# Kernel optimization log

Measured on AMD Instinct MI355X. Metric: run time of the kernel, lower is better.

## Reference

```python
import itertools
import jax, jax.numpy as jnp
import numpy as np

GRID = (41, 1600, 1408)   # KITTI voxel grid (z, y, x)
N_VOX = 80000
C_IN, C_OUT = 32, 64
NEG_SLOPE = 0.01          # nn.LeakyReLU default
BN_EPS = 1e-5

# ---------- numpy rulebook construction (spconv indice pairs) ----------

def _lin(c, grid):
    return (c[:, 0] * grid[1] + c[:, 1]) * grid[2] + c[:, 2]

def _lookup(lin_sorted, q, valid):
    pos = np.searchsorted(lin_sorted, q)
    pos = np.clip(pos, 0, len(lin_sorted) - 1)
    found = valid & (lin_sorted[pos] == q)
    return np.where(found, pos, len(lin_sorted)).astype(np.int32)  # sentinel = N

def _offsets(kshape, d):
    rs = [([-d, 0, d] if s == 3 else [0]) for s in kshape]
    return list(itertools.product(*rs))

def _subm_map(coords, lin_sorted, grid, kshape, d):
    offs = _offsets(kshape, d)
    g = np.asarray(grid)
    nbr = np.empty((len(offs), len(coords)), np.int32)
    for k, off in enumerate(offs):
        q = coords + np.asarray(off)
        valid = ((q >= 0) & (q < g)).all(1)
        nbr[k] = _lookup(lin_sorted, _lin(q, grid), valid)
    return nbr

def _build_maps(seed=0):
    rng = np.random.default_rng(seed)
    tot = GRID[0] * GRID[1] * GRID[2]
    lin0 = np.sort(rng.choice(tot, size=N_VOX, replace=False))
    c0 = np.stack(np.unravel_index(lin0, GRID), axis=1).astype(np.int64)
    nbr331_d1 = _subm_map(c0, lin0, GRID, (3, 3, 1), 1)
    nbr313_d1 = _subm_map(c0, lin0, GRID, (3, 1, 3), 1)
    # SparseConv3d k=3 s=2 p=1: output active sites = union over inputs/offsets
    og = tuple((g + 2 - 3) // 2 + 1 for g in GRID)
    offs27 = np.asarray(list(itertools.product(range(3), repeat=3)))
    cand = c0[None, :, :] + 1 - offs27[:, None, :]
    ok = (cand % 2 == 0).all(-1)
    p = cand // 2
    ok &= ((p >= 0) & (p < np.asarray(og))).all(-1)
    plin = (p[..., 0] * og[1] + p[..., 1]) * og[2] + p[..., 2]
    lin1 = np.unique(plin[ok])
    c1 = np.stack(np.unravel_index(lin1, og), axis=1).astype(np.int64)
    M = len(c1)
    pool_nbr = np.empty((27, M), np.int32)
    gg = np.asarray(GRID)
    for k in range(27):
        q = c1 * 2 - 1 + offs27[k]
        valid = ((q >= 0) & (q < gg)).all(1)
        pool_nbr[k] = _lookup(lin0, _lin(q, GRID), valid)
    nbr331_d2 = _subm_map(c1, lin1, og, (3, 3, 1), 2)
    nbr313_d2 = _subm_map(c1, lin1, og, (3, 1, 3), 2)
    nbr331_d3 = _subm_map(c1, lin1, og, (3, 3, 1), 3)
    nbr313_d3 = _subm_map(c1, lin1, og, (3, 1, 3), 3)
    maps = dict(nbr331_d1=jnp.asarray(nbr331_d1), nbr313_d1=jnp.asarray(nbr313_d1),
                pool_nbr=jnp.asarray(pool_nbr), nbr331_d2=jnp.asarray(nbr331_d2),
                nbr313_d2=jnp.asarray(nbr313_d2), nbr331_d3=jnp.asarray(nbr331_d3),
                nbr313_d3=jnp.asarray(nbr313_d3))
    return maps, M

# ---------- jax forward ----------

def _subm(f, nbr, W):
    # gather-GEMM-scatter sparse conv: out[n] = sum_k f[nbr[k,n]] @ W[k]
    padf = jnp.concatenate([f, jnp.zeros((1, f.shape[1]), f.dtype)], 0)  # zero row for missing nbr
    out = jnp.zeros((nbr.shape[1], W.shape[2]), f.dtype)
    for k in range(nbr.shape[0]):  # fixed small kernel-volume loop (9 or 27)
        out = out + padf[nbr[k]] @ W[k]
    return out

def _bn_act(x):
    # BatchNorm1d (training stats, gamma=1, beta=0 per weight_initialization) + LeakyReLU
    m = jnp.mean(x, 0)
    v = jnp.var(x, 0)
    return jax.nn.leaky_relu((x - m) * jax.lax.rsqrt(v + BN_EPS), NEG_SLOPE)

def _res(f, nA, nB, w1, w12, w2, w22):
    # nA: (3,3,1) map (conv3x1), nB: (3,1,3) map (conv1x3)
    s = _bn_act(_subm(f, nA, w1))
    s = _bn_act(_subm(s, nB, w12))
    r = _bn_act(_subm(f, nB, w2))
    r = _bn_act(_subm(r, nA, w22))
    return r + s

def setup_inputs() -> dict:
    maps, M = _build_maps()
    ks = jax.random.split(jax.random.key(0), 16)
    def w(k, shape):
        fan = shape[-2] * (shape[0] if len(shape) == 3 else 1)
        return jax.random.normal(k, shape, jnp.float32) / np.sqrt(fan)
    inp = dict(
        feats=jax.random.normal(ks[0], (N_VOX, C_IN), jnp.float32),
        b1_w1=w(ks[1], (9, C_IN, C_OUT)), b1_w1_2=w(ks[2], (9, C_OUT, C_OUT)),
        b1_w2=w(ks[3], (9, C_IN, C_OUT)), b1_w2_2=w(ks[4], (9, C_OUT, C_OUT)),
        pool_w=w(ks[5], (27, C_OUT, C_OUT)),
        b2_w1=w(ks[6], (9, C_OUT, C_OUT)), b2_w1_2=w(ks[7], (9, C_OUT, C_OUT)),
        b2_w2=w(ks[8], (9, C_OUT, C_OUT)), b2_w2_2=w(ks[9], (9, C_OUT, C_OUT)),
        b3_w1=w(ks[10], (9, C_OUT, C_OUT)), b3_w1_2=w(ks[11], (9, C_OUT, C_OUT)),
        b3_w2=w(ks[12], (9, C_OUT, C_OUT)), b3_w2_2=w(ks[13], (9, C_OUT, C_OUT)),
        down_w=w(ks[14], (3 * C_OUT, C_OUT)),
    )
    inp.update(maps)
    return inp

def reference(feats, b1_w1, b1_w1_2, b1_w2, b1_w2_2, pool_w,
              b2_w1, b2_w1_2, b2_w2, b2_w2_2,
              b3_w1, b3_w1_2, b3_w2, b3_w2_2, down_w,
              nbr331_d1, nbr313_d1, pool_nbr,
              nbr331_d2, nbr313_d2, nbr331_d3, nbr313_d3):
    x1 = _res(feats, nbr331_d1, nbr313_d1, b1_w1, b1_w1_2, b1_w2, b1_w2_2)
    x1 = _subm(x1, pool_nbr, pool_w)                     # strided SparseConv3d pool -> [M, C]
    x2 = _res(x1, nbr331_d2, nbr313_d2, b2_w1, b2_w1_2, b2_w2, b2_w2_2)  # dilation 2
    x3 = _res(x2, nbr331_d3, nbr313_d3, b3_w1, b3_w1_2, b3_w2, b3_w2_2)  # dilation 3
    return jnp.concatenate([x1, x2, x3], -1) @ down_w     # 1x1 subm conv fuse
```

## Files before the change

kernel.cpp:

```cpp
#include <hip/hip_runtime.h>
#include <hip/hip_bf16.h>

#define NEG 0.01f
#define BN_EPS 1e-5f

typedef __hip_bfloat16 bf16;
typedef __attribute__((ext_vector_type(8))) short short8;
typedef __attribute__((ext_vector_type(16))) float f32x16;

__device__ __forceinline__ float b2f(short s) {
    unsigned u = ((unsigned)(unsigned short)s) << 16;
    float f;
    __builtin_memcpy(&f, &u, 4);
    return f;
}
__device__ __forceinline__ short f2b(float f) {
    union { bf16 b; short s; } t;
    t.b = __float2bfloat16(f);
    return t.s;
}

__global__ void finalize2_k(const float* __restrict__ sA, const float* __restrict__ sB,
                            float* __restrict__ fA, float* __restrict__ fB,
                            float inv_n) {
    const float* s = blockIdx.x == 0 ? sA : sB;
    float* f = blockIdx.x == 0 ? fA : fB;
    int c = threadIdx.x;
    float sm = 0.f, sq = 0.f;
    #pragma unroll
    for (int k = 0; k < 32; ++k) {
        sm += s[k * 256 + c];
        sq += s[k * 256 + 64 + c];
    }
    float m = sm * inv_n;
    float v = sq * inv_n - m * m;
    f[c] = m;
    f[64 + c] = rsqrtf(v + BN_EPS);
}


__global__ __launch_bounds__(256) void bnact2_k(
    bf16* __restrict__ xa, const float* __restrict__ fa,
    bf16* __restrict__ xb, const float* __restrict__ fb, int nvec) {
    int i = blockIdx.x * blockDim.x + threadIdx.x;
    if (i >= 2 * nvec) return;
    bf16* x; const float* f; int j;
    if (i < nvec) { x = xa; f = fa; j = i; }
    else          { x = xb; f = fb; j = i - nvec; }
    const int c0 = (j & 7) << 3;
    short8 v = *reinterpret_cast<const short8*>(x + ((size_t)j << 3));
    short8 o;
    #pragma unroll
    for (int e = 0; e < 8; ++e) {
        float t = (b2f(v[e]) - f[c0 + e]) * f[64 + c0 + e];
        t = t > 0.f ? t : NEG * t;
        o[e] = f2b(t);
    }
    *reinterpret_cast<short8*>(x + ((size_t)j << 3)) = o;
}

__global__ __launch_bounds__(256) void bnadd_k(
    const bf16* __restrict__ a, const float* __restrict__ fa,
    const bf16* __restrict__ b, const float* __restrict__ fb,
    bf16* __restrict__ out, int nvec) {
    int i = blockIdx.x * blockDim.x + threadIdx.x;
    if (i >= nvec) return;
    const int c0 = (i & 7) << 3;
    short8 va = *reinterpret_cast<const short8*>(a + ((size_t)i << 3));
    short8 vb = *reinterpret_cast<const short8*>(b + ((size_t)i << 3));
    short8 o;
    #pragma unroll
    for (int e = 0; e < 8; ++e) {
        float ta = (b2f(va[e]) - fa[c0 + e]) * fa[64 + c0 + e];
        ta = ta > 0.f ? ta : NEG * ta;
        float tb = (b2f(vb[e]) - fb[c0 + e]) * fb[64 + c0 + e];
        tb = tb > 0.f ? tb : NEG * tb;
        o[e] = f2b(ta + tb);
    }
    *reinterpret_cast<short8*>(out + ((size_t)i << 3)) = o;
}

__global__ void cvt_f32_bf16_k(const float* __restrict__ x, bf16* __restrict__ y, int n) {
    int i = blockIdx.x * blockDim.x + threadIdx.x;
    if (i < n) y[i] = __float2bfloat16(x[i]);
}

struct PackEnt { const float* src; bf16* dst; int kt; int ns; };
struct PackArgs { PackEnt e[16]; };

__global__ void pack_w_k(PackArgs pa) {
    PackEnt E = pa.e[blockIdx.y];
    int cin = E.ns * 16;
    int total = E.kt * E.ns * 1024;
    for (int i = blockIdx.x * blockDim.x + threadIdx.x; i < total;
         i += gridDim.x * blockDim.x) {
        int j = i & 7, lane = (i >> 3) & 63, c = (i >> 9) & 1;
        int rem = i >> 10;
        int s = rem % E.ns, k = rem / E.ns;
        int krow = s * 16 + ((lane >> 5) << 3) + j;
        int col = c * 32 + (lane & 31);
        E.dst[i] = __float2bfloat16(E.src[((size_t)k * cin + krow) * 64 + col]);
    }
}

struct Job {
    const bf16* fin; const int* nbr; const bf16* Wp; bf16* out; float* stat;
    int n_out, n_in;
};
struct Jobs { Job j[2]; int t_split, t_total; };

template <int NS, int K>
__global__ __launch_bounds__(256, 6) void mconv3(Jobs jb) {
    const int CIN = NS * 16;
    const int lane = threadIdx.x & 63;
    const int col = lane & 31;
    const int q = lane >> 5;

    const int nb = gridDim.x;
    const int qq = nb >> 3, rr = nb & 7;
    const int xcd = blockIdx.x & 7, bi = blockIdx.x >> 3;
    const int sb = (xcd < rr) ? xcd * (qq + 1) + bi
                              : rr * (qq + 1) + (xcd - rr) * qq + bi;

    const int wid = sb * (blockDim.x >> 6) + (threadIdx.x >> 6);
    const int nw = gridDim.x * (blockDim.x >> 6);

    for (int tg = wid; tg < jb.t_total; tg += nw) {
        const int jsel = (tg >= jb.t_split) ? 1 : 0;
        const Job J = jb.j[jsel];
        const int tile = tg - (jsel ? jb.t_split : 0);
        const int rbase = tile << 5;
        const int r = rbase + col;
        const bool rowok = r < J.n_out;

        f32x16 acc0, acc1;
        #pragma unroll
        for (int i = 0; i < 16; ++i) { acc0[i] = 0.f; acc1[i] = 0.f; }

        #pragma unroll
        for (int g = 0; g < K / 9; ++g) {
            int idx[9];
            #pragma unroll
            for (int t = 0; t < 9; ++t)
                idx[t] = rowok ? J.nbr[(size_t)(g * 9 + t) * J.n_out + r] : J.n_in;

            #pragma unroll 1
            for (int t = 0; t < 9; ++t) {
                const bool v = idx[t] < J.n_in;
                if (__ballot(v) == 0ull) continue;
                const int k = g * 9 + t;
                const bf16* src = J.fin + (size_t)idx[t] * CIN + q * 8;
                const short8* wp = (const short8*)J.Wp + (size_t)k * (NS * 128) + lane;
                #pragma unroll
                for (int s = 0; s < NS; ++s) {
                    short8 a;
                    if (v) a = *(const short8*)(src + s * 16);
                    else { short8 z = {0,0,0,0,0,0,0,0}; a = z; }
                    short8 b0 = wp[(s * 2 + 0) * 64];
                    short8 b1 = wp[(s * 2 + 1) * 64];
                    acc0 = __builtin_amdgcn_mfma_f32_32x32x16_bf16(a, b0, acc0, 0, 0, 0);
                    acc1 = __builtin_amdgcn_mfma_f32_32x32x16_bf16(a, b1, acc1, 0, 0, 0);
                }
            }
        }

        float s0 = 0.f, q0 = 0.f, s1 = 0.f, q1 = 0.f;
        #pragma unroll
        for (int i = 0; i < 16; ++i) {
            int row = (i & 3) + 8 * (i >> 2) + 4 * q;
            int gr = rbase + row;
            if (gr < J.n_out) {
                float v0 = acc0[i], v1 = acc1[i];
                J.out[(size_t)gr * 64 + col] = __float2bfloat16(v0);
                J.out[(size_t)gr * 64 + 32 + col] = __float2bfloat16(v1);
                s0 += v0; q0 += v0 * v0;
                s1 += v1; q1 += v1 * v1;
            }
        }
        if (J.stat != nullptr) {
            s0 += __shfl_xor(s0, 32); q0 += __shfl_xor(q0, 32);
            s1 += __shfl_xor(s1, 32); q1 += __shfl_xor(q1, 32);
            float* st = J.stat + ((wid & 31) << 8);
            if (q == 0) {
                atomicAdd(&st[col], s0);
                atomicAdd(&st[64 + col], q0);
            } else {
                atomicAdd(&st[32 + col], s1);
                atomicAdd(&st[96 + col], q1);
            }
        }
    }
}

__global__ __launch_bounds__(256, 6) void down_k(
    const bf16* __restrict__ x1, const bf16* __restrict__ x2,
    const bf16* __restrict__ x3, const bf16* __restrict__ W1,
    const bf16* __restrict__ W2, const bf16* __restrict__ W3,
    float* __restrict__ out, int m) {
    const int lane = threadIdx.x & 63;
    const int col = lane & 31;
    const int q = lane >> 5;
    const int wid = blockIdx.x * (blockDim.x >> 6) + (threadIdx.x >> 6);
    const int nw = gridDim.x * (blockDim.x >> 6);
    const int ntiles = (m + 31) >> 5;

    for (int tile = wid; tile < ntiles; tile += nw) {
        const int rbase = tile << 5;
        const int r = rbase + col;
        const bool rowok = r < m;

        f32x16 acc0, acc1;
        #pragma unroll
        for (int i = 0; i < 16; ++i) { acc0[i] = 0.f; acc1[i] = 0.f; }

        const bf16* xs[3] = {x1, x2, x3};
        const bf16* ws[3] = {W1, W2, W3};
        #pragma unroll 1
        for (int t = 0; t < 3; ++t) {
            const bf16* src = xs[t] + (size_t)r * 64 + q * 8;
            const short8* wp = (const short8*)ws[t] + lane;
            #pragma unroll
            for (int s = 0; s < 4; ++s) {
                short8 a;
                if (rowok) a = *(const short8*)(src + s * 16);
                else { short8 z = {0,0,0,0,0,0,0,0}; a = z; }
                short8 b0 = wp[(s * 2 + 0) * 64];
                short8 b1 = wp[(s * 2 + 1) * 64];
                acc0 = __builtin_amdgcn_mfma_f32_32x32x16_bf16(a, b0, acc0, 0, 0, 0);
                acc1 = __builtin_amdgcn_mfma_f32_32x32x16_bf16(a, b1, acc1, 0, 0, 0);
            }
        }
        #pragma unroll
        for (int i = 0; i < 16; ++i) {
            int row = (i & 3) + 8 * (i >> 2) + 4 * q;
            int gr = rbase + row;
            if (gr < m) {
                out[(size_t)gr * 64 + col] = acc0[i];
                out[(size_t)gr * 64 + 32 + col] = acc1[i];
            }
        }
    }
}


extern "C" void kernel_launch(void* const* d_in, const int* in_sizes, int n_in_,
                              void* d_out, int out_size, void* d_ws,
                              size_t ws_size, hipStream_t stream) {
    const float* feats = (const float*)d_in[0];
    const float* Wsrc[16] = {
        (const float*)d_in[1], (const float*)d_in[2],
        (const float*)d_in[3], (const float*)d_in[4],
        (const float*)d_in[5],
        (const float*)d_in[6], (const float*)d_in[7],
        (const float*)d_in[8], (const float*)d_in[9],
        (const float*)d_in[10], (const float*)d_in[11],
        (const float*)d_in[12], (const float*)d_in[13],
        (const float*)d_in[14],
        (const float*)d_in[14] + 64 * 64,
        (const float*)d_in[14] + 128 * 64,
    };
    const int kts[16] = {9,9,9,9, 27, 9,9,9,9, 9,9,9,9, 1,1,1};
    const int nss[16] = {2,4,2,4,  4, 4,4,4,4, 4,4,4,4, 4,4,4};

    const int* nA1 = (const int*)d_in[15];
    const int* nB1 = (const int*)d_in[16];
    const int* pnbr = (const int*)d_in[17];
    const int* nA2 = (const int*)d_in[18];
    const int* nB2 = (const int*)d_in[19];
    const int* nA3 = (const int*)d_in[20];
    const int* nB3 = (const int*)d_in[21];

    const int N = in_sizes[0] / 32;
    const int M = in_sizes[17] / 27;
    const size_t MX = (size_t)(N > M ? N : M);

    bf16* A = (bf16*)d_ws;
    bf16* B = A + MX * 64;
    bf16* C = B + MX * 64;
    bf16* D = C + MX * 64;
    bf16* E = D + MX * 64;
    bf16* FB = E + MX * 64;
    bf16* WP = FB + (size_t)N * 32;
    bf16* G = (bf16*)d_out;
    bf16* Wp[16];
    {
        size_t off = 0;
        for (int i = 0; i < 16; ++i) {
            Wp[i] = WP + off;
            off += (size_t)kts[i] * nss[i] * 1024;
        }
    }
    size_t wp_total = 0;
    for (int i = 0; i < 16; ++i) wp_total += (size_t)kts[i] * nss[i] * 1024;
    float* ST = (float*)(WP + wp_total + (wp_total & 1));
    float* FS = ST + (size_t)12 * 32 * 256;
    float* out = (float*)d_out;
    auto S = [&](int i) { return ST + (size_t)i * 32 * 256; };
    auto F = [&](int i) { return FS + (size_t)i * 128; };

    hipMemsetAsync(ST, 0, (size_t)12 * 32 * 256 * sizeof(float), stream);
    {
        PackArgs pa;
        for (int i = 0; i < 16; ++i) pa.e[i] = {Wsrc[i], Wp[i], kts[i], nss[i]};
        pack_w_k<<<dim3(64, 16), 256, 0, stream>>>(pa);
    }
    cvt_f32_bf16_k<<<(N * 32 + 255) / 256, 256, 0, stream>>>(feats, FB, N * 32);

    const float invN = 1.f / (float)N, invM = 1.f / (float)M;
    const int nvN = N * 8, nvM = M * 8;

    auto mkjob = [](const bf16* fin, const int* nbr, const bf16* w, bf16* o,
                    float* st, int no, int ni) {
        Job j; j.fin = fin; j.nbr = nbr; j.Wp = w; j.out = o; j.stat = st;
        j.n_out = no; j.n_in = ni; return j;
    };
    auto pair = [&](void (*kp)(Jobs), Job a, Job b) {
        Jobs jb; jb.j[0] = a; jb.j[1] = b;
        int ta = (a.n_out + 31) >> 5, tb = (b.n_out + 31) >> 5;
        jb.t_split = ta; jb.t_total = ta + tb;
        int blocks = (jb.t_total + 3) >> 2;
        hipLaunchKernelGGL(kp, dim3(blocks), dim3(256), 0, stream, jb);
    };
    auto single = [&](void (*kp)(Jobs), Job a) {
        Jobs jb; jb.j[0] = a; jb.j[1] = a;
        int ta = (a.n_out + 31) >> 5;
        jb.t_split = ta; jb.t_total = ta;
        int blocks = (ta + 3) >> 2;
        hipLaunchKernelGGL(kp, dim3(blocks), dim3(256), 0, stream, jb);
    };

    pair(mconv3<2, 9>,
         mkjob(FB, nA1, Wp[0], A, S(0), N, N),
         mkjob(FB, nB1, Wp[2], B, S(2), N, N));
    finalize2_k<<<2, 64, 0, stream>>>(S(0), S(2), F(0), F(2), invN);
    bnact2_k<<<(2 * nvN + 255) / 256, 256, 0, stream>>>(A, F(0), B, F(2), nvN);
    pair(mconv3<4, 9>,
         mkjob(A, nB1, Wp[1], C, S(1), N, N),
         mkjob(B, nA1, Wp[3], E, S(3), N, N));
    finalize2_k<<<2, 64, 0, stream>>>(S(1), S(3), F(1), F(3), invN);
    bnadd_k<<<(nvN + 255) / 256, 256, 0, stream>>>(C, F(1), E, F(3), B, nvN);

    single(mconv3<4, 27>, mkjob(B, pnbr, Wp[4], D, nullptr, M, N));

    pair(mconv3<4, 9>,
         mkjob(D, nA2, Wp[5], A, S(4), M, M),
         mkjob(D, nB2, Wp[7], B, S(6), M, M));
    finalize2_k<<<2, 64, 0, stream>>>(S(4), S(6), F(4), F(6), invM);
    bnact2_k<<<(2 * nvM + 255) / 256, 256, 0, stream>>>(A, F(4), B, F(6), nvM);
    pair(mconv3<4, 9>,
         mkjob(A, nB2, Wp[6], C, S(5), M, M),
         mkjob(B, nA2, Wp[8], E, S(7), M, M));
    finalize2_k<<<2, 64, 0, stream>>>(S(5), S(7), F(5), F(7), invM);
    bnadd_k<<<(nvM + 255) / 256, 256, 0, stream>>>(C, F(5), E, F(7), E, nvM);

    pair(mconv3<4, 9>,
         mkjob(E, nA3, Wp[9], A, S(8), M, M),
         mkjob(E, nB3, Wp[11], B, S(10), M, M));
    finalize2_k<<<2, 64, 0, stream>>>(S(8), S(10), F(8), F(10), invM);
    bnact2_k<<<(2 * nvM + 255) / 256, 256, 0, stream>>>(A, F(8), B, F(10), nvM);
    pair(mconv3<4, 9>,
         mkjob(A, nB3, Wp[10], C, S(9), M, M),
         mkjob(B, nA3, Wp[12], G, S(11), M, M));
    finalize2_k<<<2, 64, 0, stream>>>(S(9), S(11), F(9), F(11), invM);
    bnadd_k<<<(nvM + 255) / 256, 256, 0, stream>>>(C, F(9), G, F(11), B, nvM);

    {
        int blocks = (((M + 31) >> 5) + 3) >> 2;
        down_k<<<blocks, 256, 0, stream>>>(D, E, B, Wp[13], Wp[14], Wp[15], out, M);
    }
}
```

Baseline: 669.1 us.

## Stage conv weights in LDS with persistent per-job blocks and double-buffered gathers

After: 604.9 us. 1.11x faster.

```diff
diff --git a/kernel.cpp b/kernel.cpp
--- a/kernel.cpp
+++ b/kernel.cpp
@@ -108,6 +108,113 @@
     int n_out, n_in;
 };
 struct Jobs { Job j[2]; int t_split, t_total; };
+struct Jobs4 { Job j[2]; int b_split; };
+
+template <int NS, int K>
+__global__ __launch_bounds__(512, 4) void mconv4(Jobs4 jb) {
+    __shared__ short8 WL[K * NS * 128];
+    const int CIN = NS * 16;
+    const int tid = threadIdx.x;
+    const int lane = tid & 63;
+    const int col = lane & 31;
+    const int q = lane >> 5;
+    const int widl = tid >> 6;
+    const int nwl = blockDim.x >> 6;
+
+    const int nb = gridDim.x;
+    const int qq = nb >> 3, rr = nb & 7;
+    const int xcd = blockIdx.x & 7, bi = blockIdx.x >> 3;
+    const int sb = (xcd < rr) ? xcd * (qq + 1) + bi
+                              : rr * (qq + 1) + (xcd - rr) * qq + bi;
+
+    const int jsel = (sb >= jb.b_split) ? 1 : 0;
+    const Job J = jb.j[jsel];
+    const int lb = jsel ? sb - jb.b_split : sb;
+    const int nbj = jsel ? nb - jb.b_split : jb.b_split;
+    const int ntiles = (J.n_out + 31) >> 5;
+
+    {
+        const short8* wsrc = (const short8*)J.Wp;
+        for (int i = tid; i < K * NS * 128; i += blockDim.x) WL[i] = wsrc[i];
+    }
+    __syncthreads();
+
+    const int wid = lb * nwl + widl;
+    const int nw = nbj * nwl;
+
+    for (int tile = wid; tile < ntiles; tile += nw) {
+        const int rbase = tile << 5;
+        const int r = rbase + col;
+        const bool rowok = r < J.n_out;
+
+        f32x16 acc0, acc1;
+        #pragma unroll
+        for (int i = 0; i < 16; ++i) { acc0[i] = 0.f; acc1[i] = 0.f; }
+
+        int idx[K];
+        #pragma unroll
+        for (int t = 0; t < K; ++t)
+            idx[t] = rowok ? J.nbr[(size_t)t * J.n_out + r] : J.n_in;
+
+        auto loadA = [&](int id, short8 (&dst)[NS]) {
+            const bool v = id < J.n_in;
+            const bf16* src = J.fin + (size_t)id * CIN + q * 8;
+            #pragma unroll
+            for (int s = 0; s < NS; ++s) {
+                short8 z = {0, 0, 0, 0, 0, 0, 0, 0};
+                dst[s] = z;
+                if (v) dst[s] = *(const short8*)(src + s * 16);
+            }
+        };
+        auto dotap = [&](int k, int id, short8 (&a)[NS]) {
+            if (__ballot(id < J.n_in) == 0ull) return;
+            #pragma unroll
+            for (int s = 0; s < NS; ++s) {
+                short8 b0 = WL[((k * NS + s) * 2 + 0) * 64 + lane];
+                short8 b1 = WL[((k * NS + s) * 2 + 1) * 64 + lane];
+                acc0 = __builtin_amdgcn_mfma_f32_32x32x16_bf16(a[s], b0, acc0, 0, 0, 0);
+                acc1 = __builtin_amdgcn_mfma_f32_32x32x16_bf16(a[s], b1, acc1, 0, 0, 0);
+            }
+        };
+
+        short8 A0[NS], A1[NS];
+        loadA(idx[0], A0);
+        #pragma unroll 1
+        for (int t = 0; t + 2 <= K; t += 2) {
+            loadA(idx[t + 1], A1);
+            dotap(t, idx[t], A0);
+            if (t + 2 < K) loadA(idx[t + 2], A0);
+            dotap(t + 1, idx[t + 1], A1);
+        }
+        dotap(K - 1, idx[K - 1], A0);
+
+        float s0 = 0.f, q0 = 0.f, s1 = 0.f, q1 = 0.f;
+        #pragma unroll
+        for (int i = 0; i < 16; ++i) {
+            int row = (i & 3) + 8 * (i >> 2) + 4 * q;
+            int gr = rbase + row;
+            if (gr < J.n_out) {
+                float v0 = acc0[i], v1 = acc1[i];
+                J.out[(size_t)gr * 64 + col] = __float2bfloat16(v0);
+                J.out[(size_t)gr * 64 + 32 + col] = __float2bfloat16(v1);
+                s0 += v0; q0 += v0 * v0;
+                s1 += v1; q1 += v1 * v1;
+            }
+        }
+        if (J.stat != nullptr) {
+            s0 += __shfl_xor(s0, 32); q0 += __shfl_xor(q0, 32);
+            s1 += __shfl_xor(s1, 32); q1 += __shfl_xor(q1, 32);
+            float* st = J.stat + (((sb << 3) + widl) & 31) * 256;
+            if (q == 0) {
+                atomicAdd(&st[col], s0);
+                atomicAdd(&st[64 + col], q0);
+            } else {
+                atomicAdd(&st[32 + col], s1);
+                atomicAdd(&st[96 + col], q1);
+            }
+        }
+    }
+}
 
 template <int NS, int K>
 __global__ __launch_bounds__(256, 6) void mconv3(Jobs jb) {
@@ -164,29 +271,13 @@
             }
         }
 
-        float s0 = 0.f, q0 = 0.f, s1 = 0.f, q1 = 0.f;
         #pragma unroll
         for (int i = 0; i < 16; ++i) {
             int row = (i & 3) + 8 * (i >> 2) + 4 * q;
             int gr = rbase + row;
             if (gr < J.n_out) {
-                float v0 = acc0[i], v1 = acc1[i];
-                J.out[(size_t)gr * 64 + col] = __float2bfloat16(v0);
-                J.out[(size_t)gr * 64 + 32 + col] = __float2bfloat16(v1);
-                s0 += v0; q0 += v0 * v0;
-                s1 += v1; q1 += v1 * v1;
-            }
-        }
-        if (J.stat != nullptr) {
-            s0 += __shfl_xor(s0, 32); q0 += __shfl_xor(q0, 32);
-            s1 += __shfl_xor(s1, 32); q1 += __shfl_xor(q1, 32);
-            float* st = J.stat + ((wid & 31) << 8);
-            if (q == 0) {
-                atomicAdd(&st[col], s0);
-                atomicAdd(&st[64 + col], q0);
-            } else {
-                atomicAdd(&st[32 + col], s1);
-                atomicAdd(&st[96 + col], q1);
+                J.out[(size_t)gr * 64 + col] = __float2bfloat16(acc0[i]);
+                J.out[(size_t)gr * 64 + 32 + col] = __float2bfloat16(acc1[i]);
             }
         }
     }
@@ -314,12 +405,15 @@
         Job j; j.fin = fin; j.nbr = nbr; j.Wp = w; j.out = o; j.stat = st;
         j.n_out = no; j.n_in = ni; return j;
     };
-    auto pair = [&](void (*kp)(Jobs), Job a, Job b) {
-        Jobs jb; jb.j[0] = a; jb.j[1] = b;
-        int ta = (a.n_out + 31) >> 5, tb = (b.n_out + 31) >> 5;
-        jb.t_split = ta; jb.t_total = ta + tb;
-        int blocks = (jb.t_total + 3) >> 2;
-        hipLaunchKernelGGL(kp, dim3(blocks), dim3(256), 0, stream, jb);
+    auto pair4 = [&](void (*kp)(Jobs4), Job a, Job b) {
+        Jobs4 jb; jb.j[0] = a; jb.j[1] = b;
+        const int nb = 512;
+        long ta = (a.n_out + 31) >> 5, tb = (b.n_out + 31) >> 5;
+        int bs = (int)((ta * nb + (ta + tb) / 2) / (ta + tb));
+        if (bs < 1) bs = 1;
+        if (bs > nb - 1) bs = nb - 1;
+        jb.b_split = bs;
+        hipLaunchKernelGGL(kp, dim3(nb), dim3(512), 0, stream, jb);
     };
     auto single = [&](void (*kp)(Jobs), Job a) {
         Jobs jb; jb.j[0] = a; jb.j[1] = a;
@@ -329,38 +423,38 @@
         hipLaunchKernelGGL(kp, dim3(blocks), dim3(256), 0, stream, jb);
     };
 
-    pair(mconv3<2, 9>,
-         mkjob(FB, nA1, Wp[0], A, S(0), N, N),
-         mkjob(FB, nB1, Wp[2], B, S(2), N, N));
+    pair4(mconv4<2, 9>,
+          mkjob(FB, nA1, Wp[0], A, S(0), N, N),
+          mkjob(FB, nB1, Wp[2], B, S(2), N, N));
     finalize2_k<<<2, 64, 0, stream>>>(S(0), S(2), F(0), F(2), invN);
     bnact2_k<<<(2 * nvN + 255) / 256, 256, 0, stream>>>(A, F(0), B, F(2), nvN);
-    pair(mconv3<4, 9>,
-         mkjob(A, nB1, Wp[1], C, S(1), N, N),
-         mkjob(B, nA1, Wp[3], E, S(3), N, N));
+    pair4(mconv4<4, 9>,
+          mkjob(A, nB1, Wp[1], C, S(1), N, N),
+          mkjob(B, nA1, Wp[3], E, S(3), N, N));
     finalize2_k<<<2, 64, 0, stream>>>(S(1), S(3), F(1), F(3), invN);
     bnadd_k<<<(nvN + 255) / 256, 256, 0, stream>>>(C, F(1), E, F(3), B, nvN);
 
     single(mconv3<4, 27>, mkjob(B, pnbr, Wp[4], D, nullptr, M, N));
 
-    pair(mconv3<4, 9>,
-         mkjob(D, nA2, Wp[5], A, S(4), M, M),
-         mkjob(D, nB2, Wp[7], B, S(6), M, M));
+    pair4(mconv4<4, 9>,
+          mkjob(D, nA2, Wp[5], A, S(4), M, M),
+          mkjob(D, nB2, Wp[7], B, S(6), M, M));
     finalize2_k<<<2, 64, 0, stream>>>(S(4), S(6), F(4), F(6), invM);
     bnact2_k<<<(2 * nvM + 255) / 256, 256, 0, stream>>>(A, F(4), B, F(6), nvM);
-    pair(mconv3<4, 9>,
-         mkjob(A, nB2, Wp[6], C, S(5), M, M),
-         mkjob(B, nA2, Wp[8], E, S(7), M, M));
+    pair4(mconv4<4, 9>,
+          mkjob(A, nB2, Wp[6], C, S(5), M, M),
+          mkjob(B, nA2, Wp[8], E, S(7), M, M));
     finalize2_k<<<2, 64, 0, stream>>>(S(5), S(7), F(5), F(7), invM);
     bnadd_k<<<(nvM + 255) / 256, 256, 0, stream>>>(C, F(5), E, F(7), E, nvM);
 
-    pair(mconv3<4, 9>,
-         mkjob(E, nA3, Wp[9], A, S(8), M, M),
-         mkjob(E, nB3, Wp[11], B, S(10), M, M));
+    pair4(mconv4<4, 9>,
+          mkjob(E, nA3, Wp[9], A, S(8), M, M),
+          mkjob(E, nB3, Wp[11], B, S(10), M, M));
     finalize2_k<<<2, 64, 0, stream>>>(S(8), S(10), F(8), F(10), invM);
     bnact2_k<<<(2 * nvM + 255) / 256, 256, 0, stream>>>(A, F(8), B, F(10), nvM);
-    pair(mconv3<4, 9>,
-         mkjob(A, nB3, Wp[10], C, S(9), M, M),
-         mkjob(B, nA3, Wp[12], G, S(11), M, M));
+    pair4(mconv4<4, 9>,
+          mkjob(A, nB3, Wp[10], C, S(9), M, M),
+          mkjob(B, nA3, Wp[12], G, S(11), M, M));
     finalize2_k<<<2, 64, 0, stream>>>(S(9), S(11), F(9), F(11), invM);
     bnadd_k<<<(nvM + 255) / 256, 256, 0, stream>>>(C, F(9), G, F(11), B, nvM);
 
```
